# Performance work log

Hardware: AMD Instinct MI355X
Metric: run time of the kernel (lower is better)

The kernel has to match this reference:

```python
import jax, jax.numpy as jnp
import numpy as np

N = 100000
E = 3200000
IN_DIM = 128
HD = 64
HEADS = 4
NEG_SLOPE = 0.2


def setup_inputs() -> dict:
    key = jax.random.key(0)
    ks = jax.random.split(key, 12)
    s = lambda fan_in: 1.0 / np.sqrt(fan_in)
    x = jax.random.normal(ks[0], (N, IN_DIM), dtype=jnp.float32)
    edge_index = jax.random.randint(ks[1], (2, E), 0, N, dtype=jnp.int64)
    W1 = jax.random.normal(ks[2], (IN_DIM, HEADS * HD), dtype=jnp.float32) * s(IN_DIM)
    a_src1 = jax.random.normal(ks[3], (HEADS, HD), dtype=jnp.float32) * s(HD)
    a_dst1 = jax.random.normal(ks[4], (HEADS, HD), dtype=jnp.float32) * s(HD)
    b1 = jnp.zeros((HEADS * HD,), dtype=jnp.float32)
    W2 = jax.random.normal(ks[5], (HEADS * HD, HD), dtype=jnp.float32) * s(HEADS * HD)
    a_src2 = jax.random.normal(ks[6], (1, HD), dtype=jnp.float32) * s(HD)
    a_dst2 = jax.random.normal(ks[7], (1, HD), dtype=jnp.float32) * s(HD)
    b2 = jnp.zeros((HD,), dtype=jnp.float32)
    lin_w = jax.random.normal(ks[8], (HD, 2), dtype=jnp.float32) * s(HD)
    lin_b = jnp.zeros((2,), dtype=jnp.float32)
    return {"x": x, "edge_index": edge_index, "W1": W1, "a_src1": a_src1,
            "a_dst1": a_dst1, "b1": b1, "W2": W2, "a_src2": a_src2,
            "a_dst2": a_dst2, "b2": b2, "lin_w": lin_w, "lin_b": lin_b}


def gat_conv(x, src, dst, W, a_src, a_dst, bias, heads, out_dim, concat):
    n = x.shape[0]
    h = (x @ W).reshape(n, heads, out_dim)                 # [N,H,D]
    alpha_s = jnp.einsum('nhd,hd->nh', h, a_src)           # [N,H]
    alpha_d = jnp.einsum('nhd,hd->nh', h, a_dst)           # [N,H]
    e = alpha_s[src] + alpha_d[dst]                        # [Etot,H]
    e = jnp.where(e > 0, e, NEG_SLOPE * e)                 # leaky relu
    m = jax.ops.segment_max(e, dst, num_segments=n)        # scatter-softmax (stable)
    m = jnp.where(jnp.isfinite(m), m, 0.0)
    e = jnp.exp(e - m[dst])
    denom = jax.ops.segment_sum(e, dst, num_segments=n)
    alpha = e / denom[dst]                                 # [Etot,H]
    out = jax.ops.segment_sum(h[src] * alpha[:, :, None], dst, num_segments=n)  # [N,H,D]
    out = out.reshape(n, heads * out_dim) if concat else out.mean(axis=1)
    return out + bias


def reference(x, edge_index, W1, a_src1, a_dst1, b1, W2, a_src2, a_dst2, b2, lin_w, lin_b):
    n = x.shape[0]
    loops = jnp.arange(n, dtype=edge_index.dtype)
    src = jnp.concatenate([edge_index[0], loops])          # add self-loops (PyG default)
    dst = jnp.concatenate([edge_index[1], loops])
    h = gat_conv(x, src, dst, W1, a_src1, a_dst1, b1, HEADS, HD, True)
    h = jax.nn.elu(h)
    h = gat_conv(h, src, dst, W2, a_src2, a_dst2, b2, 1, HD, True)
    h = jax.nn.elu(h)
    return h @ lin_w + lin_b                               # [N,2]
```

## Files before the change

### kernel.cpp

```cpp
#include <hip/hip_runtime.h>
#include <hip/hip_fp16.h>
#include <math.h>

#define NN 100000
#define EE 3200000
#define ETOT (EE + NN)
#define NEG_SLOPE 0.2f
#define DMAX 96
#define CHUNK 4096
#define NB0 ((ETOT + CHUNK - 1) / CHUNK)
#define RB 391
#define CAP 16384
#define PREPB 391

typedef _Float16 half8 __attribute__((ext_vector_type(8)));
typedef _Float16 half4v __attribute__((ext_vector_type(4)));
typedef _Float16 half2v __attribute__((ext_vector_type(2)));
typedef float floatx4 __attribute__((ext_vector_type(4)));

__device__ __forceinline__ float wsum64(float v) {
#pragma unroll
  for (int o = 32; o; o >>= 1) v += __shfl_xor(v, o);
  return v;
}
__device__ __forceinline__ float lrelu(float v) { return v > 0.f ? v : NEG_SLOPE * v; }
__device__ __forceinline__ float elu1(float v) { return v > 0.f ? v : expm1f(v); }

__global__ void k_init(int* __restrict__ ccur) {
  ccur[threadIdx.x] = threadIdx.x * CAP;
}

__global__ __launch_bounds__(256) void k_pass1(const int* __restrict__ ei,
                                               int* __restrict__ ccur,
                                               unsigned* __restrict__ ebuf,
                                               const float* __restrict__ W1,
                                               const float* __restrict__ W2,
                                               _Float16* __restrict__ W1t,
                                               _Float16* __restrict__ W2t,
                                               const float* __restrict__ x,
                                               const float* __restrict__ a_src1,
                                               const float* __restrict__ a_dst1,
                                               _Float16* __restrict__ xh,
                                               float* __restrict__ as1,
                                               float* __restrict__ ad1) {
  __shared__ __align__(16) char smem[26624];
  const int b = blockIdx.x;
  const int t = threadIdx.x;
  if (b < NB0) {
    unsigned* vv = (unsigned*)smem;
    unsigned short* cbv = (unsigned short*)(smem + 16384);
    int* h = (int*)(smem + 24576);
    int* cur = (int*)(smem + 25600);
    h[t] = 0;
    __syncthreads();
    int base = b * CHUNK;
    int lim = base + CHUNK; if (lim > ETOT) lim = ETOT;
    int cnt = lim - base;
    for (int i = t; i < cnt; i += 256) {
      int e = base + i;
      int s, d;
      if (e < EE) { s = ei[e]; d = ei[EE + e]; } else { s = e - EE; d = s; }
      unsigned cb = (unsigned)d / (unsigned)RB;
      unsigned dloc = (unsigned)d - cb * (unsigned)RB;
      vv[i] = (dloc << 17) | (unsigned)s;
      cbv[i] = (unsigned short)cb;
      atomicAdd(&h[cb], 1);
    }
    __syncthreads();
    if (h[t]) cur[t] = atomicAdd(&ccur[t], h[t]);
    __syncthreads();
    for (int i = t; i < cnt; i += 256) {
      int cb = cbv[i];
      int pos = atomicAdd(&cur[cb], 1);
      ebuf[pos] = vv[i];
    }
    return;
  }
  if (b < NB0 + 192) {
    int idx = (b - NB0) * 256 + t;
    if (idx < 32768) {
      int n = idx >> 7, k = idx & 127;
      W1t[idx] = (_Float16)W1[k * 256 + n];
    } else {
      int j = idx - 32768;
      int n = j >> 8, k = j & 255;
      W2t[j] = (_Float16)W2[k * 64 + n];
    }
    return;
  }
  float* vs = (float*)smem;
  float* vd = vs + 512;
  for (int i = t; i < 512; i += 256) {
    int h = i >> 7, k = i & 127;
    const float* wrow = W1 + (size_t)k * 256 + h * 64;
    float ss = 0.f, dd = 0.f;
#pragma unroll 8
    for (int d2 = 0; d2 < 64; ++d2) {
      float wv = wrow[d2];
      ss = fmaf(wv, a_src1[h * 64 + d2], ss);
      dd = fmaf(wv, a_dst1[h * 64 + d2], dd);
    }
    vs[i] = ss; vd[i] = dd;
  }
  __syncthreads();
  const int lane = t & 63;
  const int gw = (b - NB0 - 192) * 4 + (t >> 6);
  for (int n = gw; n < NN; n += 4 * PREPB) {
    float2 xv = *(const float2*)(x + (size_t)n * 128 + lane * 2);
    half2v hx; hx[0] = (_Float16)xv.x; hx[1] = (_Float16)xv.y;
    *(half2v*)(xh + (size_t)n * 128 + lane * 2) = hx;
    float p[8];
#pragma unroll
    for (int h = 0; h < 4; ++h) {
      p[h]     = xv.x * vs[h * 128 + lane * 2] + xv.y * vs[h * 128 + lane * 2 + 1];
      p[4 + h] = xv.x * vd[h * 128 + lane * 2] + xv.y * vd[h * 128 + lane * 2 + 1];
    }
#pragma unroll
    for (int j = 0; j < 8; ++j) p[j] = wsum64(p[j]);
    if (lane == 0) {
      *(float4*)(as1 + n * 4) = make_float4(p[0], p[1], p[2], p[3]);
      *(float4*)(ad1 + n * 4) = make_float4(p[4], p[5], p[6], p[7]);
    }
  }
}

__global__ __launch_bounds__(256) void k_pass2(const unsigned* __restrict__ ebuf,
                                               const int* __restrict__ ccur,
                                               int* __restrict__ offs,
                                               int* __restrict__ degarr,
                                               int* __restrict__ csr) {
  __shared__ unsigned ed[CAP];
  __shared__ int hist[RB];
  __shared__ int cur[RB];
  int b = blockIdx.x, t = threadIdx.x;
  int d0 = b * RB;
  int rb = NN - d0; if (rb > RB) rb = RB;
  int w0 = b * CAP;
  int cnt = ccur[b] - w0;
  if (cnt > CAP) cnt = CAP;
  for (int j = t; j < rb; j += 256) hist[j] = 0;
  __syncthreads();
  for (int i = t; i < cnt; i += 256) {
    unsigned v = ebuf[w0 + i];
    ed[i] = v;
    atomicAdd(&hist[v >> 17], 1);
  }
  __syncthreads();
  if (t == 0) {
    int run = w0;
    for (int j = 0; j < rb; ++j) { cur[j] = run; run += hist[j]; }
  }
  __syncthreads();
  for (int j = t; j < rb; j += 256) {
    offs[d0 + j] = cur[j];
    degarr[d0 + j] = hist[j];
  }
  __syncthreads();
  for (int i = t; i < cnt; i += 256) {
    unsigned v = ed[i];
    int pos = atomicAdd(&cur[v >> 17], 1);
    csr[pos] = (int)(v & 0x1FFFFu);
  }
}

__global__ __launch_bounds__(256) void k_fused1(const int* __restrict__ offs,
                                                const int* __restrict__ degarr,
                                                const int* __restrict__ csr_src,
                                                const float* __restrict__ a_s,
                                                const float* __restrict__ a_d,
                                                const _Float16* __restrict__ xh,
                                                const _Float16* __restrict__ W1t,
                                                const _Float16* __restrict__ W2t,
                                                const float* __restrict__ b1,
                                                const float* __restrict__ a_src2,
                                                const float* __restrict__ a_dst2,
                                                _Float16* __restrict__ h2h,
                                                float* __restrict__ as_out,
                                                float* __restrict__ ad_out) {
  __shared__ __align__(16) float alp[4][DMAX][4];
  __shared__ int sidx[4][DMAX];
  __shared__ __align__(16) _Float16 aggT[16][520];
  __shared__ __align__(16) _Float16 h1eT[16][264];
  __shared__ float prt[2][4][16];
  const int wid = threadIdx.x >> 6;
  const int lane = threadIdx.x & 63;
  const int n0 = blockIdx.x * 16;
  const int g = lane >> 4;
  const int sub = lane & 15;
  const _Float16* __restrict__ hb = xh + sub * 8;

  for (int dn = 0; dn < 4; ++dn) {
    const int n = n0 + wid * 4 + dn;
    const int beg = offs[n], deg = degarr[n];
    const float4 ad = *(const float4*)(a_d + n * 4);
    float4 sm = make_float4(0.f, 0.f, 0.f, 0.f);
    for (int d = lane; d < deg; d += 64) {
      int s = csr_src[beg + d];
      float4 as = *(const float4*)(a_s + s * 4);
      float e0 = __expf(lrelu(as.x + ad.x));
      float e1 = __expf(lrelu(as.y + ad.y));
      float e2 = __expf(lrelu(as.z + ad.z));
      float e3 = __expf(lrelu(as.w + ad.w));
      sm.x += e0; sm.y += e1; sm.z += e2; sm.w += e3;
      if (d < DMAX) {
        sidx[wid][d] = s;
        *(float4*)&alp[wid][d][0] = make_float4(e0, e1, e2, e3);
      }
    }
    sm.x = wsum64(sm.x); sm.y = wsum64(sm.y); sm.z = wsum64(sm.z); sm.w = wsum64(sm.w);
    const float4 inv4 = make_float4(1.f / sm.x, 1.f / sm.y, 1.f / sm.z, 1.f / sm.w);
    const int dlim = deg < DMAX ? deg : DMAX;
    for (int d = lane; d < dlim; d += 64) {
      float4 a = *(float4*)&alp[wid][d][0];
      a.x *= inv4.x; a.y *= inv4.y; a.z *= inv4.z; a.w *= inv4.w;
      *(float4*)&alp[wid][d][0] = a;
    }
    float acc[4][8];
#pragma unroll
    for (int h = 0; h < 4; ++h)
#pragma unroll
      for (int j = 0; j < 8; ++j) acc[h][j] = 0.f;
    int d = 0;
    for (; d + 8 <= dlim; d += 8) {
      int i0 = d + g, i1 = d + 4 + g;
      int s0 = sidx[wid][i0], s1 = sidx[wid][i1];
      float4 w0 = *(float4*)&alp[wid][i0][0];
      float4 w1 = *(float4*)&alp[wid][i1][0];
      half8 r0 = *(const half8*)(hb + (size_t)s0 * 128);
      half8 r1 = *(const half8*)(hb + (size_t)s1 * 128);
#pragma unroll
      for (int j = 0; j < 8; ++j) {
        float f0 = (float)r0[j], f1 = (float)r1[j];
        acc[0][j] = fmaf(f0, w0.x, acc[0][j]);
        acc[1][j] = fmaf(f0, w0.y, acc[1][j]);
        acc[2][j] = fmaf(f0, w0.z, acc[2][j]);
        acc[3][j] = fmaf(f0, w0.w, acc[3][j]);
        acc[0][j] = fmaf(f1, w1.x, acc[0][j]);
        acc[1][j] = fmaf(f1, w1.y, acc[1][j]);
        acc[2][j] = fmaf(f1, w1.z, acc[2][j]);
        acc[3][j] = fmaf(f1, w1.w, acc[3][j]);
      }
    }
    if (d + 4 <= dlim) {
      int i0 = d + g;
      int s0 = sidx[wid][i0];
      float4 w0 = *(float4*)&alp[wid][i0][0];
      half8 r0 = *(const half8*)(hb + (size_t)s0 * 128);
#pragma unroll
      for (int j = 0; j < 8; ++j) {
        float f0 = (float)r0[j];
        acc[0][j] = fmaf(f0, w0.x, acc[0][j]);
        acc[1][j] = fmaf(f0, w0.y, acc[1][j]);
        acc[2][j] = fmaf(f0, w0.z, acc[2][j]);
        acc[3][j] = fmaf(f0, w0.w, acc[3][j]);
      }
      d += 4;
    }
    if (d < dlim) {
      int idx = d + g;
      bool v = idx < dlim;
      int s = sidx[wid][v ? idx : d];
      float4 w0 = *(float4*)&alp[wid][v ? idx : d][0];
      if (!v) { w0.x = 0.f; w0.y = 0.f; w0.z = 0.f; w0.w = 0.f; }
      half8 r0 = *(const half8*)(hb + (size_t)s * 128);
#pragma unroll
      for (int j = 0; j < 8; ++j) {
        float f0 = (float)r0[j];
        acc[0][j] = fmaf(f0, w0.x, acc[0][j]);
        acc[1][j] = fmaf(f0, w0.y, acc[1][j]);
        acc[2][j] = fmaf(f0, w0.z, acc[2][j]);
        acc[3][j] = fmaf(f0, w0.w, acc[3][j]);
      }
    }
    if (deg > DMAX) {
      for (int dd = DMAX + g; dd < deg; dd += 4) {
        int s = csr_src[beg + dd];
        float4 as = *(const float4*)(a_s + s * 4);
        float w0x = __expf(lrelu(as.x + ad.x)) * inv4.x;
        float w0y = __expf(lrelu(as.y + ad.y)) * inv4.y;
        float w0z = __expf(lrelu(as.z + ad.z)) * inv4.z;
        float w0w = __expf(lrelu(as.w + ad.w)) * inv4.w;
        half8 r0 = *(const half8*)(hb + (size_t)s * 128);
#pragma unroll
        for (int j = 0; j < 8; ++j) {
          float f0 = (float)r0[j];
          acc[0][j] = fmaf(f0, w0x, acc[0][j]);
          acc[1][j] = fmaf(f0, w0y, acc[1][j]);
          acc[2][j] = fmaf(f0, w0z, acc[2][j]);
          acc[3][j] = fmaf(f0, w0w, acc[3][j]);
        }
      }
    }
#pragma unroll
    for (int h = 0; h < 4; ++h)
#pragma unroll
      for (int j = 0; j < 8; ++j) {
        acc[h][j] += __shfl_xor(acc[h][j], 16);
        acc[h][j] += __shfl_xor(acc[h][j], 32);
      }
    if (g == 0) {
#pragma unroll
      for (int h = 0; h < 4; ++h) {
        half8 o;
#pragma unroll
        for (int j = 0; j < 8; ++j) o[j] = (_Float16)acc[h][j];
        *(half8*)&aggT[wid * 4 + dn][h * 128 + sub * 8] = o;
      }
    }
  }
  __syncthreads();

  const int m16 = sub, quad = g;
  floatx4 acc1[4];
#pragma unroll
  for (int nt = 0; nt < 4; ++nt) acc1[nt] = (floatx4){0.f, 0.f, 0.f, 0.f};
#pragma unroll
  for (int ks = 0; ks < 4; ++ks) {
    half8 av = *(half8*)&aggT[m16][wid * 128 + ks * 32 + quad * 8];
#pragma unroll
    for (int nt = 0; nt < 4; ++nt) {
      half8 bv = *(const half8*)(W1t + (size_t)(wid * 64 + nt * 16 + m16) * 128 + ks * 32 + quad * 8);
      acc1[nt] = __builtin_amdgcn_mfma_f32_16x16x32_f16(av, bv, acc1[nt], 0, 0, 0);
    }
  }
#pragma unroll
  for (int nt = 0; nt < 4; ++nt) {
    float bb = b1[wid * 64 + nt * 16 + m16];
#pragma unroll
    for (int r = 0; r < 4; ++r)
      h1eT[quad * 4 + r][wid * 64 + nt * 16 + m16] = (_Float16)elu1(acc1[nt][r] + bb);
  }
  __syncthreads();

  floatx4 acc2 = (floatx4){0.f, 0.f, 0.f, 0.f};
#pragma unroll
  for (int ks = 0; ks < 8; ++ks) {
    half8 av = *(half8*)&h1eT[m16][ks * 32 + quad * 8];
    half8 bv = *(const half8*)(W2t + (size_t)(wid * 16 + m16) * 256 + ks * 32 + quad * 8);
    acc2 = __builtin_amdgcn_mfma_f32_16x16x32_f16(av, bv, acc2, 0, 0, 0);
  }
  const float a2v = a_src2[wid * 16 + m16];
  const float d2v = a_dst2[wid * 16 + m16];
#pragma unroll
  for (int r = 0; r < 4; ++r) {
    int row = quad * 4 + r;
    h2h[(size_t)(n0 + row) * 64 + wid * 16 + m16] = (_Float16)acc2[r];
    float ps = acc2[r] * a2v, pd = acc2[r] * d2v;
#pragma unroll
    for (int o = 1; o < 16; o <<= 1) { ps += __shfl_xor(ps, o); pd += __shfl_xor(pd, o); }
    if (m16 == 0) { prt[0][wid][row] = ps; prt[1][wid][row] = pd; }
  }
  __syncthreads();
  if (threadIdx.x < 16) {
    int row = threadIdx.x;
    as_out[n0 + row] = prt[0][0][row] + prt[0][1][row] + prt[0][2][row] + prt[0][3][row];
    ad_out[n0 + row] = prt[1][0][row] + prt[1][1][row] + prt[1][2][row] + prt[1][3][row];
  }
}

__global__ __launch_bounds__(256) void k_attn2(const int* __restrict__ offs,
                                               const int* __restrict__ degarr,
                                               const int* __restrict__ csr_src,
                                               const float* __restrict__ a_s,
                                               const float* __restrict__ a_d,
                                               const _Float16* __restrict__ h2h,
                                               const float* __restrict__ b2,
                                               const float* __restrict__ lin_w,
                                               const float* __restrict__ lin_b,
                                               float* __restrict__ out) {
  __shared__ float alpha2[4][DMAX];
  __shared__ int sidx2[4][DMAX];
  const int wid = threadIdx.x >> 6;
  const int n = blockIdx.x * 4 + wid;
  const int lane = threadIdx.x & 63;
  const int beg = offs[n], deg = degarr[n];
  const float adn = a_d[n];
  float sm = 0.f;
  for (int d = lane; d < deg; d += 64) {
    int s = csr_src[beg + d];
    float e = __expf(lrelu(a_s[s] + adn));
    sm += e;
    if (d < DMAX) { sidx2[wid][d] = s; alpha2[wid][d] = e; }
  }
  sm = wsum64(sm);
  const float inv = 1.f / sm;
  const int dlim = deg < DMAX ? deg : DMAX;
  for (int d = lane; d < dlim; d += 64) alpha2[wid][d] *= inv;
  const int g = lane >> 4;
  const int sub = lane & 15;
  const _Float16* __restrict__ hb = h2h + sub * 4;
  float a0 = 0.f, a1 = 0.f, a2 = 0.f, a3 = 0.f;
  int d = 0;
  for (; d + 8 <= dlim; d += 8) {
    int i0 = d + g, i1 = d + 4 + g;
    int s0 = sidx2[wid][i0], s1 = sidx2[wid][i1];
    float w0 = alpha2[wid][i0], w1 = alpha2[wid][i1];
    half4v r0 = *(const half4v*)(hb + (size_t)s0 * 64);
    half4v r1 = *(const half4v*)(hb + (size_t)s1 * 64);
    a0 = fmaf((float)r0[0], w0, a0); a1 = fmaf((float)r0[1], w0, a1);
    a2 = fmaf((float)r0[2], w0, a2); a3 = fmaf((float)r0[3], w0, a3);
    a0 = fmaf((float)r1[0], w1, a0); a1 = fmaf((float)r1[1], w1, a1);
    a2 = fmaf((float)r1[2], w1, a2); a3 = fmaf((float)r1[3], w1, a3);
  }
  if (d + 4 <= dlim) {
    int i0 = d + g;
    int s0 = sidx2[wid][i0];
    float w0 = alpha2[wid][i0];
    half4v r0 = *(const half4v*)(hb + (size_t)s0 * 64);
    a0 = fmaf((float)r0[0], w0, a0); a1 = fmaf((float)r0[1], w0, a1);
    a2 = fmaf((float)r0[2], w0, a2); a3 = fmaf((float)r0[3], w0, a3);
    d += 4;
  }
  if (d < dlim) {
    int idx = d + g;
    bool v = idx < dlim;
    int s = sidx2[wid][v ? idx : d];
    float w = v ? alpha2[wid][idx] : 0.f;
    half4v r = *(const half4v*)(hb + (size_t)s * 64);
    a0 = fmaf((float)r[0], w, a0); a1 = fmaf((float)r[1], w, a1);
    a2 = fmaf((float)r[2], w, a2); a3 = fmaf((float)r[3], w, a3);
  }
  if (deg > DMAX && g == 0) {
    for (int dd = DMAX; dd < deg; ++dd) {
      int s = csr_src[beg + dd];
      float w = __expf(lrelu(a_s[s] + adn)) * inv;
      half4v r = *(const half4v*)(hb + (size_t)s * 64);
      a0 = fmaf((float)r[0], w, a0); a1 = fmaf((float)r[1], w, a1);
      a2 = fmaf((float)r[2], w, a2); a3 = fmaf((float)r[3], w, a3);
    }
  }
  a0 += __shfl_xor(a0, 16); a1 += __shfl_xor(a1, 16);
  a2 += __shfl_xor(a2, 16); a3 += __shfl_xor(a3, 16);
  a0 += __shfl_xor(a0, 32); a1 += __shfl_xor(a1, 32);
  a2 += __shfl_xor(a2, 32); a3 += __shfl_xor(a3, 32);
  const int c = sub * 4;
  float4 bb = *(const float4*)(b2 + c);
  float o0 = elu1(a0 + bb.x);
  float o1 = elu1(a1 + bb.y);
  float o2 = elu1(a2 + bb.z);
  float o3 = elu1(a3 + bb.w);
  float4 lw0 = *(const float4*)(lin_w + c * 2);
  float4 lw1 = *(const float4*)(lin_w + c * 2 + 4);
  float p0 = o0 * lw0.x + o1 * lw0.z + o2 * lw1.x + o3 * lw1.z;
  float p1 = o0 * lw0.y + o1 * lw0.w + o2 * lw1.y + o3 * lw1.w;
  p0 = wsum64(p0) * 0.25f;
  p1 = wsum64(p1) * 0.25f;
  if (lane == 0) {
    out[n * 2 + 0] = p0 + lin_b[0];
    out[n * 2 + 1] = p1 + lin_b[1];
  }
}

extern "C" void kernel_launch(void* const* d_in, const int* in_sizes, int n_in,
                              void* d_out, int out_size, void* d_ws, size_t ws_size,
                              hipStream_t stream) {
  const float* x      = (const float*)d_in[0];
  const int*   ei     = (const int*)d_in[1];
  const float* W1     = (const float*)d_in[2];
  const float* a_src1 = (const float*)d_in[3];
  const float* a_dst1 = (const float*)d_in[4];
  const float* b1     = (const float*)d_in[5];
  const float* W2     = (const float*)d_in[6];
  const float* a_src2 = (const float*)d_in[7];
  const float* a_dst2 = (const float*)d_in[8];
  const float* b2     = (const float*)d_in[9];
  const float* lin_w  = (const float*)d_in[10];
  const float* lin_b  = (const float*)d_in[11];
  float* outp = (float*)d_out;

  char* w = (char*)d_ws;
  _Float16* xh   = (_Float16*)(w + 0);
  _Float16* h2h  = (_Float16*)(w + 25600000);
  unsigned* ebuf = (unsigned*)(w + 38400000);
  int*    csr    = (int*)(w + 55177216);
  _Float16* W1t  = (_Float16*)(w + 71954432);
  _Float16* W2t  = (_Float16*)(w + 72019968);
  float*  as1    = (float*)(w + 72052736);
  float*  ad1    = (float*)(w + 73652736);
  float*  as2    = (float*)(w + 75252736);
  float*  ad2    = (float*)(w + 75652736);
  int*    offs   = (int*)(w + 76052736);
  int*    degarr = (int*)(w + 76452736);
  int*    ccur   = (int*)(w + 76852736);

  k_init<<<1, 256, 0, stream>>>(ccur);
  k_pass1<<<NB0 + 192 + PREPB, 256, 0, stream>>>(ei, ccur, ebuf, W1, W2, W1t, W2t,
                                                 x, a_src1, a_dst1, xh, as1, ad1);
  k_pass2<<<256, 256, 0, stream>>>(ebuf, ccur, offs, degarr, csr);

  k_fused1<<<NN / 16, 256, 0, stream>>>(offs, degarr, csr, as1, ad1, xh,
                                        W1t, W2t, b1, a_src2, a_dst2, h2h, as2, ad2);

  k_attn2<<<NN / 4, 256, 0, stream>>>(offs, degarr, csr, as2, ad2, h2h, b2, lin_w, lin_b, outp);
}
```

Before: 551.7 us.

## Use one wave per destination node in fused layer-1 kernel with 1024-thread blocks

The fused layer-1 kernel now launches 1024-thread blocks with 16 waves, one per destination node, where before 4 waves each looped over 4 nodes serially. The first MFMA GEMM is split so each of the 16 waves computes one 16x16 output tile. Only 4 waves run the second GEMM. The aim is more memory-level parallelism during the irregular gather. In exchange, LDS use per block grows, 1024-thread blocks may limit occupancy and scheduling, and 12 waves sit idle during the second GEMM.

```diff
diff --git a/kernel.cpp b/kernel.cpp
--- a/kernel.cpp
+++ b/kernel.cpp
@@ -163,22 +163,22 @@
   }
 }
 
-__global__ __launch_bounds__(256) void k_fused1(const int* __restrict__ offs,
-                                                const int* __restrict__ degarr,
-                                                const int* __restrict__ csr_src,
-                                                const float* __restrict__ a_s,
-                                                const float* __restrict__ a_d,
-                                                const _Float16* __restrict__ xh,
-                                                const _Float16* __restrict__ W1t,
-                                                const _Float16* __restrict__ W2t,
-                                                const float* __restrict__ b1,
-                                                const float* __restrict__ a_src2,
-                                                const float* __restrict__ a_dst2,
-                                                _Float16* __restrict__ h2h,
-                                                float* __restrict__ as_out,
-                                                float* __restrict__ ad_out) {
-  __shared__ __align__(16) float alp[4][DMAX][4];
-  __shared__ int sidx[4][DMAX];
+__global__ __launch_bounds__(1024) void k_fused16(const int* __restrict__ offs,
+                                                  const int* __restrict__ degarr,
+                                                  const int* __restrict__ csr_src,
+                                                  const float* __restrict__ a_s,
+                                                  const float* __restrict__ a_d,
+                                                  const _Float16* __restrict__ xh,
+                                                  const _Float16* __restrict__ W1t,
+                                                  const _Float16* __restrict__ W2t,
+                                                  const float* __restrict__ b1,
+                                                  const float* __restrict__ a_src2,
+                                                  const float* __restrict__ a_dst2,
+                                                  _Float16* __restrict__ h2h,
+                                                  float* __restrict__ as_out,
+                                                  float* __restrict__ ad_out) {
+  __shared__ __align__(16) float alp[16][DMAX][4];
+  __shared__ int sidx[16][DMAX];
   __shared__ __align__(16) _Float16 aggT[16][520];
   __shared__ __align__(16) _Float16 h1eT[16][264];
   __shared__ float prt[2][4][16];
@@ -189,8 +189,8 @@
   const int sub = lane & 15;
   const _Float16* __restrict__ hb = xh + sub * 8;
 
-  for (int dn = 0; dn < 4; ++dn) {
-    const int n = n0 + wid * 4 + dn;
+  {
+    const int n = n0 + wid;
     const int beg = offs[n], deg = degarr[n];
     const float4 ad = *(const float4*)(a_d + n * 4);
     float4 sm = make_float4(0.f, 0.f, 0.f, 0.f);
@@ -304,51 +304,48 @@
         half8 o;
 #pragma unroll
         for (int j = 0; j < 8; ++j) o[j] = (_Float16)acc[h][j];
-        *(half8*)&aggT[wid * 4 + dn][h * 128 + sub * 8] = o;
+        *(half8*)&aggT[wid][h * 128 + sub * 8] = o;
       }
     }
   }
   __syncthreads();
 
   const int m16 = sub, quad = g;
-  floatx4 acc1[4];
-#pragma unroll
-  for (int nt = 0; nt < 4; ++nt) acc1[nt] = (floatx4){0.f, 0.f, 0.f, 0.f};
+  const int hB = wid >> 2, ntB = wid & 3;
+  floatx4 acc1 = (floatx4){0.f, 0.f, 0.f, 0.f};
 #pragma unroll
   for (int ks = 0; ks < 4; ++ks) {
-    half8 av = *(half8*)&aggT[m16][wid * 128 + ks * 32 + quad * 8];
-#pragma unroll
-    for (int nt = 0; nt < 4; ++nt) {
-      half8 bv = *(const half8*)(W1t + (size_t)(wid * 64 + nt * 16 + m16) * 128 + ks * 32 + quad * 8);
-      acc1[nt] = __builtin_amdgcn_mfma_f32_16x16x32_f16(av, bv, acc1[nt], 0, 0, 0);
-    }
-  }
-#pragma unroll
-  for (int nt = 0; nt < 4; ++nt) {
-    float bb = b1[wid * 64 + nt * 16 + m16];
+    half8 av = *(half8*)&aggT[m16][hB * 128 + ks * 32 + quad * 8];
+    half8 bv = *(const half8*)(W1t + (size_t)(hB * 64 + ntB * 16 + m16) * 128 + ks * 32 + quad * 8);
+    acc1 = __builtin_amdgcn_mfma_f32_16x16x32_f16(av, bv, acc1, 0, 0, 0);
+  }
+  {
+    float bb = b1[hB * 64 + ntB * 16 + m16];
 #pragma unroll
     for (int r = 0; r < 4; ++r)
-      h1eT[quad * 4 + r][wid * 64 + nt * 16 + m16] = (_Float16)elu1(acc1[nt][r] + bb);
-  }
-  __syncthreads();
-
-  floatx4 acc2 = (floatx4){0.f, 0.f, 0.f, 0.f};
-#pragma unroll
-  for (int ks = 0; ks < 8; ++ks) {
-    half8 av = *(half8*)&h1eT[m16][ks * 32 + quad * 8];
-    half8 bv = *(const half8*)(W2t + (size_t)(wid * 16 + m16) * 256 + ks * 32 + quad * 8);
-    acc2 = __builtin_amdgcn_mfma_f32_16x16x32_f16(av, bv, acc2, 0, 0, 0);
-  }
-  const float a2v = a_src2[wid * 16 + m16];
-  const float d2v = a_dst2[wid * 16 + m16];
-#pragma unroll
-  for (int r = 0; r < 4; ++r) {
-    int row = quad * 4 + r;
-    h2h[(size_t)(n0 + row) * 64 + wid * 16 + m16] = (_Float16)acc2[r];
-    float ps = acc2[r] * a2v, pd = acc2[r] * d2v;
-#pragma unroll
-    for (int o = 1; o < 16; o <<= 1) { ps += __shfl_xor(ps, o); pd += __shfl_xor(pd, o); }
-    if (m16 == 0) { prt[0][wid][row] = ps; prt[1][wid][row] = pd; }
+      h1eT[quad * 4 + r][hB * 64 + ntB * 16 + m16] = (_Float16)elu1(acc1[r] + bb);
+  }
+  __syncthreads();
+
+  if (wid < 4) {
+    floatx4 acc2 = (floatx4){0.f, 0.f, 0.f, 0.f};
+#pragma unroll
+    for (int ks = 0; ks < 8; ++ks) {
+      half8 av = *(half8*)&h1eT[m16][ks * 32 + quad * 8];
+      half8 bv = *(const half8*)(W2t + (size_t)(wid * 16 + m16) * 256 + ks * 32 + quad * 8);
+      acc2 = __builtin_amdgcn_mfma_f32_16x16x32_f16(av, bv, acc2, 0, 0, 0);
+    }
+    const float a2v = a_src2[wid * 16 + m16];
+    const float d2v = a_dst2[wid * 16 + m16];
+#pragma unroll
+    for (int r = 0; r < 4; ++r) {
+      int row = quad * 4 + r;
+      h2h[(size_t)(n0 + row) * 64 + wid * 16 + m16] = (_Float16)acc2[r];
+      float ps = acc2[r] * a2v, pd = acc2[r] * d2v;
+#pragma unroll
+      for (int o = 1; o < 16; o <<= 1) { ps += __shfl_xor(ps, o); pd += __shfl_xor(pd, o); }
+      if (m16 == 0) { prt[0][wid][row] = ps; prt[1][wid][row] = pd; }
+    }
   }
   __syncthreads();
   if (threadIdx.x < 16) {
@@ -488,8 +485,8 @@
                                                  x, a_src1, a_dst1, xh, as1, ad1);
   k_pass2<<<256, 256, 0, stream>>>(ebuf, ccur, offs, degarr, csr);
 
-  k_fused1<<<NN / 16, 256, 0, stream>>>(offs, degarr, csr, as1, ad1, xh,
-                                        W1t, W2t, b1, a_src2, a_dst2, h2h, as2, ad2);
+  k_fused16<<<NN / 16, 1024, 0, stream>>>(offs, degarr, csr, as1, ad1, xh,
+                                          W1t, W2t, b1, a_src2, a_dst2, h2h, as2, ad2);
 
   k_attn2<<<NN / 4, 256, 0, stream>>>(offs, degarr, csr, as2, ad2, h2h, b2, lin_w, lin_b, outp);
 }
```

After: 627.1 us. 13.7% more time.
